# Optimization experiments

Hardware: AMD Instinct MI355X
Metric: run time of the kernel (lower is better)

Reference implementation:

```python
import jax, jax.numpy as jnp
import numpy as np


def setup_inputs() -> dict:
    key = jax.random.key(0)
    ks = jax.random.split(key, 5)
    B, S, H, I = 8, 2048, 1024, 4096
    # int8 quantized activation / weights / int8 bias, held as int32 for portability
    hidden_states = jax.random.randint(ks[0], (B, S, H), -128, 128, dtype=jnp.int32)
    w_fc = jax.random.randint(ks[1], (H, I), -128, 128, dtype=jnp.int32)   # Conv1D weight [in, out]
    b_fc = jax.random.randint(ks[2], (I,), -128, 128, dtype=jnp.int32)     # int8 bias (B8)
    w_proj = jax.random.randint(ks[3], (I, H), -128, 128, dtype=jnp.int32)
    b_proj = jax.random.normal(ks[4], (H,), dtype=jnp.float32)             # fp32 bias (BFP32)
    alpha_fc = jnp.float32(0.004)   # (x_scale * w_scale / out_scale) of c_fc
    beta_fc = jnp.float32(0.02)     # bias_scale / out_scale of c_fc
    alpha_proj = jnp.float32(0.003) # x_scale * w_scale of c_proj (dequant to fp32)
    return {
        "hidden_states": hidden_states,
        "w_fc": w_fc, "b_fc": b_fc, "alpha_fc": alpha_fc, "beta_fc": beta_fc,
        "w_proj": w_proj, "b_proj": b_proj, "alpha_proj": alpha_proj,
    }


def reference(hidden_states, w_fc, b_fc, alpha_fc, beta_fc, w_proj, b_proj, alpha_proj):
    # ---- c_fc: W8A8B8O8 Conv1D + fused ReLU + requantization to int8 ----
    acc1 = jnp.matmul(hidden_states, w_fc)                       # [B,S,I] int32
    h = acc1.astype(jnp.float32) * alpha_fc + b_fc.astype(jnp.float32) * beta_fc
    h = jax.nn.relu(h)
    # requantize to int8 (round + saturate)
    h_q = jnp.clip(jnp.round(h), -128.0, 127.0).astype(jnp.int32)  # [B,S,I]
    # ---- c_proj: W8A8BFP32OFP32 Conv1D (dequant to fp32) ----
    acc2 = jnp.matmul(h_q, w_proj)                               # [B,S,H] int32
    out = acc2.astype(jnp.float32) * alpha_proj + b_proj
    # dropout is identity in eval mode
    return out
```

## Files before the change

### kernel.cpp

```cpp
#include <hip/hip_runtime.h>
#include <cstdint>
#include <cstddef>

typedef int int4v __attribute__((ext_vector_type(4)));
typedef signed char schar;

#define DEVI __device__ __forceinline__

DEVI void load_lds16(const void* g, void* l) {
  __builtin_amdgcn_global_load_lds(
      (const __attribute__((address_space(1))) void*)g,
      (__attribute__((address_space(3))) void*)l, 16, 0, 0);
}

#define BAR() __builtin_amdgcn_s_barrier()
#define LGKM(n) asm volatile("s_waitcnt lgkmcnt(" #n ")")
#define VMW(n) asm volatile("s_waitcnt vmcnt(" #n ")")

__global__ __launch_bounds__(256) void pack_i8(const int* __restrict__ src,
                                               signed char* __restrict__ dst,
                                               int n4) {
  int i = blockIdx.x * 256 + threadIdx.x;
  if (i >= n4) return;
  int4v v = ((const int4v*)src)[i];
  int p = (v.x & 255) | ((v.y & 255) << 8) | ((v.z & 255) << 16) | (v.w << 24);
  ((int*)dst)[i] = p;
}

__global__ __launch_bounds__(256) void pack_wT(const int* __restrict__ w,
                                               signed char* __restrict__ wT,
                                               int K, int N) {
  __shared__ signed char t[64][68];
  int n0 = blockIdx.x * 64, k0 = blockIdx.y * 64;
  int tr = threadIdx.x >> 6, tc = threadIdx.x & 63;
#pragma unroll
  for (int i = 0; i < 16; ++i) {
    int r = i * 4 + tr;
    t[r][tc] = (signed char)w[(size_t)(k0 + r) * N + n0 + tc];
  }
  __syncthreads();
#pragma unroll
  for (int i = 0; i < 16; ++i) {
    int r = i * 4 + tr;
    wT[(size_t)(n0 + r) * K + k0 + tc] = t[tc][r];
  }
}

template <int EPI>
__global__ __launch_bounds__(1024, 4) void gemmV(
    const schar* __restrict__ A, const schar* __restrict__ BT,
    int M, int N, int K, const int* __restrict__ bias_i,
    const float* __restrict__ alphaP, const float* __restrict__ betaP,
    const float* __restrict__ bias_f, schar* __restrict__ outQ,
    float* __restrict__ outF) {
  extern __shared__ schar lds[];

  const int tid = threadIdx.x;
  const int wid = tid >> 6, lane = tid & 63;
  const int wr = wid >> 2, wc = wid & 3;
  const int l16 = lane & 15, l4 = lane >> 4;

  const int gx = gridDim.x;
  const int nwg = gx * gridDim.y;
  const int bid = blockIdx.y * gx + blockIdx.x;
  const int swz = (bid & 7) * (nwg >> 3) + (bid >> 3);
  const int rowBase = (swz / gx) * 256;
  const int colBase = (swz % gx) * 256;
  const int NT = K >> 6;

  const float alpha = alphaP[0];
  const float beta = (EPI == 0) ? betaP[0] : 0.f;
  asm volatile("" ::"s"(alpha), "s"(beta));
  LGKM(0);

  const int o = tid * 16;
  const int rr = o >> 6;
  const int gsl = ((o >> 4) & 3) ^ ((rr >> 1) & 3);
  const schar* gAs = A + (size_t)(rowBase + rr) * K + gsl * 16;
  const schar* gBs = BT + (size_t)(colBase + rr) * K + gsl * 16;

  auto stage = [&](int buf, int t) {
    schar* d = lds + buf * 32768 + wid * 1024;
    load_lds16(gAs + (size_t)t * 64, d);
    load_lds16(gBs + (size_t)t * 64, d + 16384);
  };

  const int slotc = (l4 ^ ((l16 >> 1) & 3)) * 16 + l16 * 64;
  const int aoff = wr * 4096 + slotc;
  const int boff = 16384 + wc * 4096 + slotc;

  int4v acc[4][4] = {};
  int4v aF[4], bF[4];

#define RDT(Bu)                                                    \
  do {                                                             \
    _Pragma("unroll") for (int mi = 0; mi < 4; ++mi) aF[mi] =      \
        *(const int4v*)((Bu) + aoff + mi * 1024);                  \
    _Pragma("unroll") for (int ni = 0; ni < 4; ++ni) bF[ni] =      \
        *(const int4v*)((Bu) + boff + ni * 1024);                  \
  } while (0)
#define MMT()                                                          \
  do {                                                                 \
    __builtin_amdgcn_s_setprio(1);                                     \
    _Pragma("unroll") for (int mi = 0; mi < 4; ++mi)                   \
        _Pragma("unroll") for (int ni = 0; ni < 4; ++ni) acc[mi][ni] = \
        __builtin_amdgcn_mfma_i32_16x16x64_i8(aF[mi], bF[ni],          \
                                              acc[mi][ni], 0, 0, 0);   \
    __builtin_amdgcn_s_setprio(0);                                     \
  } while (0)

  stage(0, 0);
  stage(1, 1);
  VMW(0);
  BAR();

  for (int T = 0; T < NT; T += 2) {
    if (T + 2 < NT) stage((T + 2) & 3, T + 2);
    if (T + 3 < NT) stage((T + 3) & 3, T + 3);

    RDT(lds + (T & 3) * 32768);
    MMT();
    RDT(lds + ((T + 1) & 3) * 32768);
    MMT();

    LGKM(0);
    VMW(0);
    BAR();
  }

  if (EPI == 0) {
#pragma unroll
    for (int MI = 0; MI < 4; ++MI) {
      int row = rowBase + wr * 64 + MI * 16 + l4 * 4;
#pragma unroll
      for (int NI = 0; NI < 4; ++NI) {
        int col = colBase + wc * 64 + NI * 16 + l16;
        float bt = (float)bias_i[col] * beta;
#pragma unroll
        for (int j = 0; j < 4; ++j) {
          float h = (float)acc[MI][NI][j] * alpha + bt;
          h = fmaxf(h, 0.f);
          h = rintf(h);
          h = fminf(h, 127.f);
          outQ[(size_t)(row + j) * N + col] = (schar)h;
        }
      }
    }
  } else {
#pragma unroll
    for (int MI = 0; MI < 4; ++MI) {
      int row = rowBase + wr * 64 + MI * 16 + l4 * 4;
#pragma unroll
      for (int NI = 0; NI < 4; ++NI) {
        int col = colBase + wc * 64 + NI * 16 + l16;
        float bv = bias_f[col];
#pragma unroll
        for (int j = 0; j < 4; ++j)
          outF[(size_t)(row + j) * N + col] =
              (float)acc[MI][NI][j] * alpha + bv;
      }
    }
  }
#undef RDT
#undef MMT
}

extern "C" void kernel_launch(void* const* d_in, const int* in_sizes, int n_in,
                              void* d_out, int out_size, void* d_ws,
                              size_t ws_size, hipStream_t stream) {
  const int M = 16384, H = 1024, I = 4096;
  const int* hidden = (const int*)d_in[0];
  const int* w_fc = (const int*)d_in[1];
  const int* b_fc = (const int*)d_in[2];
  const float* alpha_fc = (const float*)d_in[3];
  const float* beta_fc = (const float*)d_in[4];
  const int* w_proj = (const int*)d_in[5];
  const float* b_proj = (const float*)d_in[6];
  const float* alpha_proj = (const float*)d_in[7];
  float* out = (float*)d_out;

  signed char* hq = (signed char*)d_ws;
  signed char* aP = hq + (size_t)M * I;
  signed char* wfcT = aP + (size_t)M * H;
  signed char* wpT = wfcT + (size_t)I * H;

  hipFuncSetAttribute((const void*)gemmV<0>,
                      hipFuncAttributeMaxDynamicSharedMemorySize, 131072);
  hipFuncSetAttribute((const void*)gemmV<1>,
                      hipFuncAttributeMaxDynamicSharedMemorySize, 131072);

  pack_i8<<<(M * H / 4 + 255) / 256, 256, 0, stream>>>(hidden, aP, M * H / 4);
  pack_wT<<<dim3(I / 64, H / 64), 256, 0, stream>>>(w_fc, wfcT, H, I);
  pack_wT<<<dim3(H / 64, I / 64), 256, 0, stream>>>(w_proj, wpT, I, H);

  gemmV<0><<<dim3(I / 256, M / 256), 1024, 131072, stream>>>(
      aP, wfcT, M, I, H, b_fc, alpha_fc, beta_fc, nullptr, hq, nullptr);
  gemmV<1><<<dim3(H / 256, M / 256), 1024, 131072, stream>>>(
      hq, wpT, M, H, I, nullptr, alpha_proj, nullptr, b_proj, nullptr, out);
}
```

Measured before the change: 177.6 us.

## Use 4-wave blocks with 128x128 per-wave tiles and K=128 double buffering

The GEMM kernel moves from 16 waves per block with 64x64 warp tiles to 4 waves per block, each computing a 128x128 sub-tile of the same 256x256 block tile. The K step grows from 64 to 128, and the 4-stage pipeline becomes a 2-stage double buffer with an 8-way XOR swizzle. The aim is more MFMA work per LDS fragment load and fewer barriers. The cost is a 64-register accumulator array plus 16 fragment registers per lane, heavy VGPR/AGPR pressure, fewer waves to hide latency, and less prefetch depth.

New measurement: 214.5 us. 20.8% more time.

```diff
diff --git a/kernel.cpp b/kernel.cpp
--- a/kernel.cpp
+++ b/kernel.cpp
@@ -47,7 +47,7 @@
 }
 
 template <int EPI>
-__global__ __launch_bounds__(1024, 4) void gemmV(
+__global__ __launch_bounds__(256, 1) void gemmX(
     const schar* __restrict__ A, const schar* __restrict__ BT,
     int M, int N, int K, const int* __restrict__ bias_i,
     const float* __restrict__ alphaP, const float* __restrict__ betaP,
@@ -57,7 +57,7 @@
 
   const int tid = threadIdx.x;
   const int wid = tid >> 6, lane = tid & 63;
-  const int wr = wid >> 2, wc = wid & 3;
+  const int wr = wid >> 1, wc = wid & 1;
   const int l16 = lane & 15, l4 = lane >> 4;
 
   const int gx = gridDim.x;
@@ -66,62 +66,68 @@
   const int swz = (bid & 7) * (nwg >> 3) + (bid >> 3);
   const int rowBase = (swz / gx) * 256;
   const int colBase = (swz % gx) * 256;
-  const int NT = K >> 6;
+  const int NT = K >> 7;
 
   const float alpha = alphaP[0];
   const float beta = (EPI == 0) ? betaP[0] : 0.f;
   asm volatile("" ::"s"(alpha), "s"(beta));
   LGKM(0);
 
-  const int o = tid * 16;
-  const int rr = o >> 6;
-  const int gsl = ((o >> 4) & 3) ^ ((rr >> 1) & 3);
-  const schar* gAs = A + (size_t)(rowBase + rr) * K + gsl * 16;
-  const schar* gBs = BT + (size_t)(colBase + rr) * K + gsl * 16;
+  const int strow = tid >> 3;
+  const int gs = (tid & 7) ^ (strow & 7);
+  const schar* gA0 = A + (size_t)(rowBase + strow) * K + gs * 16;
+  const schar* gB0 = BT + (size_t)(colBase + strow) * K + gs * 16;
+  const size_t cstep = (size_t)32 * K;
 
   auto stage = [&](int buf, int t) {
-    schar* d = lds + buf * 32768 + wid * 1024;
-    load_lds16(gAs + (size_t)t * 64, d);
-    load_lds16(gBs + (size_t)t * 64, d + 16384);
+    schar* dA = lds + buf * 65536 + wid * 1024;
+    schar* dB = dA + 32768;
+#pragma unroll
+    for (int c = 0; c < 8; ++c)
+      load_lds16(gA0 + (size_t)t * 128 + c * cstep, dA + c * 4096);
+#pragma unroll
+    for (int c = 0; c < 8; ++c)
+      load_lds16(gB0 + (size_t)t * 128 + c * cstep, dB + c * 4096);
   };
 
-  const int slotc = (l4 ^ ((l16 >> 1) & 3)) * 16 + l16 * 64;
-  const int aoff = wr * 4096 + slotc;
-  const int boff = 16384 + wc * 4096 + slotc;
-
-  int4v acc[4][4] = {};
-  int4v aF[4], bF[4];
-
-#define RDT(Bu)                                                    \
+  const int so0 = ((0 + l4) ^ (l16 & 7)) * 16 + l16 * 128;
+  const int so1 = ((4 + l4) ^ (l16 & 7)) * 16 + l16 * 128;
+  const int aoff = wr * 16384;
+  const int boff = 32768 + wc * 16384;
+
+  int4v acc[8][8] = {};
+  int4v aF[8], bF[8];
+
+#define RDK(SO, Bu)                                                \
   do {                                                             \
-    _Pragma("unroll") for (int mi = 0; mi < 4; ++mi) aF[mi] =      \
-        *(const int4v*)((Bu) + aoff + mi * 1024);                  \
-    _Pragma("unroll") for (int ni = 0; ni < 4; ++ni) bF[ni] =      \
-        *(const int4v*)((Bu) + boff + ni * 1024);                  \
+    _Pragma("unroll") for (int f = 0; f < 8; ++f) aF[f] =          \
+        *(const int4v*)((Bu) + aoff + f * 2048 + (SO));            \
+    _Pragma("unroll") for (int f = 0; f < 8; ++f) bF[f] =          \
+        *(const int4v*)((Bu) + boff + f * 2048 + (SO));            \
   } while (0)
-#define MMT()                                                          \
+#define MMK()                                                          \
   do {                                                                 \
     __builtin_amdgcn_s_setprio(1);                                     \
-    _Pragma("unroll") for (int mi = 0; mi < 4; ++mi)                   \
-        _Pragma("unroll") for (int ni = 0; ni < 4; ++ni) acc[mi][ni] = \
+    _Pragma("unroll") for (int mi = 0; mi < 8; ++mi)                   \
+        _Pragma("unroll") for (int ni = 0; ni < 8; ++ni) acc[mi][ni] = \
         __builtin_amdgcn_mfma_i32_16x16x64_i8(aF[mi], bF[ni],          \
                                               acc[mi][ni], 0, 0, 0);   \
     __builtin_amdgcn_s_setprio(0);                                     \
   } while (0)
 
   stage(0, 0);
-  stage(1, 1);
   VMW(0);
   BAR();
 
-  for (int T = 0; T < NT; T += 2) {
-    if (T + 2 < NT) stage((T + 2) & 3, T + 2);
-    if (T + 3 < NT) stage((T + 3) & 3, T + 3);
-
-    RDT(lds + (T & 3) * 32768);
-    MMT();
-    RDT(lds + ((T + 1) & 3) * 32768);
-    MMT();
+  for (int T = 0; T < NT; ++T) {
+    const schar* Bu = lds + (T & 1) * 65536;
+
+    if (T + 1 < NT) stage((T + 1) & 1, T + 1);
+
+    RDK(so0, Bu);
+    MMK();
+    RDK(so1, Bu);
+    MMK();
 
     LGKM(0);
     VMW(0);
@@ -130,11 +136,11 @@
 
   if (EPI == 0) {
 #pragma unroll
-    for (int MI = 0; MI < 4; ++MI) {
-      int row = rowBase + wr * 64 + MI * 16 + l4 * 4;
-#pragma unroll
-      for (int NI = 0; NI < 4; ++NI) {
-        int col = colBase + wc * 64 + NI * 16 + l16;
+    for (int MI = 0; MI < 8; ++MI) {
+      int row = rowBase + wr * 128 + MI * 16 + l4 * 4;
+#pragma unroll
+      for (int NI = 0; NI < 8; ++NI) {
+        int col = colBase + wc * 128 + NI * 16 + l16;
         float bt = (float)bias_i[col] * beta;
 #pragma unroll
         for (int j = 0; j < 4; ++j) {
@@ -148,11 +154,11 @@
     }
   } else {
 #pragma unroll
-    for (int MI = 0; MI < 4; ++MI) {
-      int row = rowBase + wr * 64 + MI * 16 + l4 * 4;
-#pragma unroll
-      for (int NI = 0; NI < 4; ++NI) {
-        int col = colBase + wc * 64 + NI * 16 + l16;
+    for (int MI = 0; MI < 8; ++MI) {
+      int row = rowBase + wr * 128 + MI * 16 + l4 * 4;
+#pragma unroll
+      for (int NI = 0; NI < 8; ++NI) {
+        int col = colBase + wc * 128 + NI * 16 + l16;
         float bv = bias_f[col];
 #pragma unroll
         for (int j = 0; j < 4; ++j)
@@ -161,8 +167,8 @@
       }
     }
   }
-#undef RDT
-#undef MMT
+#undef RDK
+#undef MMK
 }
 
 extern "C" void kernel_launch(void* const* d_in, const int* in_sizes, int n_in,
@@ -184,17 +190,17 @@
   signed char* wfcT = aP + (size_t)M * H;
   signed char* wpT = wfcT + (size_t)I * H;
 
-  hipFuncSetAttribute((const void*)gemmV<0>,
+  hipFuncSetAttribute((const void*)gemmX<0>,
                       hipFuncAttributeMaxDynamicSharedMemorySize, 131072);
-  hipFuncSetAttribute((const void*)gemmV<1>,
+  hipFuncSetAttribute((const void*)gemmX<1>,
                       hipFuncAttributeMaxDynamicSharedMemorySize, 131072);
 
   pack_i8<<<(M * H / 4 + 255) / 256, 256, 0, stream>>>(hidden, aP, M * H / 4);
   pack_wT<<<dim3(I / 64, H / 64), 256, 0, stream>>>(w_fc, wfcT, H, I);
   pack_wT<<<dim3(H / 64, I / 64), 256, 0, stream>>>(w_proj, wpT, I, H);
 
-  gemmV<0><<<dim3(I / 256, M / 256), 1024, 131072, stream>>>(
+  gemmX<0><<<dim3(I / 256, M / 256), 256, 131072, stream>>>(
       aP, wfcT, M, I, H, b_fc, alpha_fc, beta_fc, nullptr, hq, nullptr);
-  gemmV<1><<<dim3(H / 256, M / 256), 1024, 131072, stream>>>(
+  gemmX<1><<<dim3(H / 256, M / 256), 256, 131072, stream>>>(
       hq, wpT, M, H, I, nullptr, alpha_proj, nullptr, b_proj, nullptr, out);
 }
```

## Shrink GEMM tile to 128x256 with 512 threads and double buffering

Applied to the files above, without the earlier changes.

Changes the int8 GEMM block tile from 256x256 with 1024 threads to 128x256 with 512 threads. The LDS pipeline drops from a 4-stage to a 2-stage buffer, using 48KB of LDS instead of 128KB. The loop now processes one K-tile per barrier instead of two, and the MFMA priority bumps are removed. The aim is to fit more workgroups per CU and get more blocks for load balance, at the cost of less operand reuse per tile and shallower prefetch.

New measurement: 189.2 us. 6.5% more time.

```diff
diff --git a/kernel.cpp b/kernel.cpp
--- a/kernel.cpp
+++ b/kernel.cpp
@@ -47,7 +47,7 @@
 }
 
 template <int EPI>
-__global__ __launch_bounds__(1024, 4) void gemmV(
+__global__ __launch_bounds__(512, 4) void gemmI(
     const schar* __restrict__ A, const schar* __restrict__ BT,
     int M, int N, int K, const int* __restrict__ bias_i,
     const float* __restrict__ alphaP, const float* __restrict__ betaP,
@@ -64,7 +64,7 @@
   const int nwg = gx * gridDim.y;
   const int bid = blockIdx.y * gx + blockIdx.x;
   const int swz = (bid & 7) * (nwg >> 3) + (bid >> 3);
-  const int rowBase = (swz / gx) * 256;
+  const int rowBase = (swz / gx) * 128;
   const int colBase = (swz % gx) * 256;
   const int NT = K >> 6;
 
@@ -73,21 +73,29 @@
   asm volatile("" ::"s"(alpha), "s"(beta));
   LGKM(0);
 
-  const int o = tid * 16;
-  const int rr = o >> 6;
-  const int gsl = ((o >> 4) & 3) ^ ((rr >> 1) & 3);
-  const schar* gAs = A + (size_t)(rowBase + rr) * K + gsl * 16;
-  const schar* gBs = BT + (size_t)(colBase + rr) * K + gsl * 16;
+  const int oA = tid * 16;
+  const int rA = oA >> 6;
+  const int gA_ = ((oA >> 4) & 3) ^ ((rA >> 1) & 3);
+  const schar* gAs = A + (size_t)(rowBase + rA) * K + gA_ * 16;
+  const schar* gBs[2];
+#pragma unroll
+  for (int c = 0; c < 2; ++c) {
+    int o = c * 8192 + tid * 16;
+    int r = o >> 6;
+    int g = ((o >> 4) & 3) ^ ((r >> 1) & 3);
+    gBs[c] = BT + (size_t)(colBase + r) * K + g * 16;
+  }
 
   auto stage = [&](int buf, int t) {
-    schar* d = lds + buf * 32768 + wid * 1024;
+    schar* d = lds + buf * 24576 + wid * 1024;
     load_lds16(gAs + (size_t)t * 64, d);
-    load_lds16(gBs + (size_t)t * 64, d + 16384);
+    load_lds16(gBs[0] + (size_t)t * 64, d + 8192);
+    load_lds16(gBs[1] + (size_t)t * 64, d + 16384);
   };
 
   const int slotc = (l4 ^ ((l16 >> 1) & 3)) * 16 + l16 * 64;
   const int aoff = wr * 4096 + slotc;
-  const int boff = 16384 + wc * 4096 + slotc;
+  const int boff = 8192 + wc * 4096 + slotc;
 
   int4v acc[4][4] = {};
   int4v aF[4], bF[4];
@@ -100,27 +108,21 @@
         *(const int4v*)((Bu) + boff + ni * 1024);                  \
   } while (0)
 #define MMT()                                                          \
-  do {                                                                 \
-    __builtin_amdgcn_s_setprio(1);                                     \
-    _Pragma("unroll") for (int mi = 0; mi < 4; ++mi)                   \
-        _Pragma("unroll") for (int ni = 0; ni < 4; ++ni) acc[mi][ni] = \
-        __builtin_amdgcn_mfma_i32_16x16x64_i8(aF[mi], bF[ni],          \
-                                              acc[mi][ni], 0, 0, 0);   \
-    __builtin_amdgcn_s_setprio(0);                                     \
-  } while (0)
+  _Pragma("unroll") for (int mi = 0; mi < 4; ++mi)                     \
+      _Pragma("unroll") for (int ni = 0; ni < 4; ++ni) acc[mi][ni] =   \
+      __builtin_amdgcn_mfma_i32_16x16x64_i8(aF[mi], bF[ni],            \
+                                            acc[mi][ni], 0, 0, 0)
 
   stage(0, 0);
-  stage(1, 1);
   VMW(0);
   BAR();
 
-  for (int T = 0; T < NT; T += 2) {
-    if (T + 2 < NT) stage((T + 2) & 3, T + 2);
-    if (T + 3 < NT) stage((T + 3) & 3, T + 3);
+  for (int T = 0; T < NT; ++T) {
+    const schar* Bu = lds + (T & 1) * 24576;
 
-    RDT(lds + (T & 3) * 32768);
-    MMT();
-    RDT(lds + ((T + 1) & 3) * 32768);
+    if (T + 1 < NT) stage((T + 1) & 1, T + 1);
+
+    RDT(Bu);
     MMT();
 
     LGKM(0);
@@ -184,17 +186,12 @@
   signed char* wfcT = aP + (size_t)M * H;
   signed char* wpT = wfcT + (size_t)I * H;
 
-  hipFuncSetAttribute((const void*)gemmV<0>,
-                      hipFuncAttributeMaxDynamicSharedMemorySize, 131072);
-  hipFuncSetAttribute((const void*)gemmV<1>,
-                      hipFuncAttributeMaxDynamicSharedMemorySize, 131072);
-
   pack_i8<<<(M * H / 4 + 255) / 256, 256, 0, stream>>>(hidden, aP, M * H / 4);
   pack_wT<<<dim3(I / 64, H / 64), 256, 0, stream>>>(w_fc, wfcT, H, I);
   pack_wT<<<dim3(H / 64, I / 64), 256, 0, stream>>>(w_proj, wpT, I, H);
 
-  gemmV<0><<<dim3(I / 256, M / 256), 1024, 131072, stream>>>(
+  gemmI<0><<<dim3(I / 256, M / 128), 512, 49152, stream>>>(
       aP, wfcT, M, I, H, b_fc, alpha_fc, beta_fc, nullptr, hq, nullptr);
-  gemmV<1><<<dim3(H / 256, M / 256), 1024, 131072, stream>>>(
+  gemmI<1><<<dim3(H / 256, M / 128), 512, 49152, stream>>>(
       hq, wpT, M, H, I, nullptr, alpha_proj, nullptr, b_proj, nullptr, out);
 }
```
